# Performance work log

Hardware: AMD Instinct MI355X
Metric: run time of the kernel (lower is better)

## Reference

```python
import jax, jax.numpy as jnp
import numpy as np

B, S, D, H = 2, 2048, 1024, 16
DK = D // H


def setup_inputs() -> dict:
    key = jax.random.key(0)
    ks = jax.random.split(key, 12)
    sc = 1.0 / np.sqrt(D)
    return {
        "q": jax.random.normal(ks[0], (B, S, D), jnp.float32),
        "k": jax.random.normal(ks[1], (B, S, D), jnp.float32),
        "v": jax.random.normal(ks[2], (B, S, D), jnp.float32),
        "mask": jax.random.randint(ks[3], (B, S), 0, 2, jnp.int32),
        "Wq": jax.random.normal(ks[4], (D, D), jnp.float32) * sc,
        "bq": jnp.zeros((D,), jnp.float32),
        "Wk": jax.random.normal(ks[5], (D, D), jnp.float32) * sc,
        "bk": jnp.zeros((D,), jnp.float32),
        "Wv": jax.random.normal(ks[6], (D, D), jnp.float32) * sc,
        "bv": jnp.zeros((D,), jnp.float32),
        "Wo": jax.random.normal(ks[7], (D, D), jnp.float32) * sc,
        "bo": jnp.zeros((D,), jnp.float32),
    }


def reference(q, k, v, mask, Wq, bq, Wk, bk, Wv, bv, Wo, bo):
    # Projections (flax nn.Dense: x @ W + b)
    query = q @ Wq + bq          # [B,S,D]
    key_ = k @ Wk + bk
    value = v @ Wv + bv
    # split heads -> [B,H,S,DK]
    def split(x):
        return x.reshape(B, S, H, DK).transpose(0, 2, 1, 3)
    qh, kh, vh = split(query), split(key_), split(value)
    scores = jnp.einsum('bhqd,bhkd->bhqk', qh, kh) / jnp.sqrt(jnp.float32(DK))
    # Faithful to source: mask=(mask==0); where(mask==0, -1e10, scores)
    # i.e. positions where ORIGINAL mask != 0 are set to -1e10.
    m = (mask == 0)[:, None, None, :]          # [B,1,1,S] bool
    scores = jnp.where(~m, jnp.float32(-1e10), scores)
    attn = jax.nn.softmax(scores, axis=-1)     # dropout deterministic (eval)
    x = jnp.einsum('bhqk,bhkd->bhqd', attn, vh)
    x = x.transpose(0, 2, 1, 3).reshape(B, S, D)
    return x @ Wo + bo
```

## Files before the change

### kernel.cpp

```cpp
#include <hip/hip_runtime.h>
#include <hip/hip_bf16.h>

typedef unsigned short u16;
typedef unsigned int u32;
typedef __attribute__((ext_vector_type(8))) __bf16 bf16x8;
typedef __attribute__((ext_vector_type(4))) float f32x4;
typedef __attribute__((ext_vector_type(16))) float f32x16;

constexpr int Bz = 2, Sq = 2048, Dm = 1024, Hn = 16, DK = 64;

__device__ __forceinline__ u16 f2bf(float f) {
    u32 u = __builtin_bit_cast(u32, f);
    return (u16)((u + 0x7FFFu + ((u >> 16) & 1u)) >> 16);
}

__device__ __forceinline__ u32 pack_bf16(float a, float b) {
#if __has_builtin(__builtin_amdgcn_cvt_pk_bf16_f32)
    return __builtin_bit_cast(u32, __builtin_amdgcn_cvt_pk_bf16_f32(a, b));
#else
    return (u32)f2bf(a) | ((u32)f2bf(b) << 16);
#endif
}

__device__ __forceinline__ bf16x8 lds_frag(const u16* p) {
    return __builtin_bit_cast(bf16x8, *(const uint4*)p);
}
__device__ __forceinline__ bf16x8 gfrag(const u16* p) {
    return __builtin_bit_cast(bf16x8, *(const uint4*)p);
}
__device__ __forceinline__ int swz(int r) { return (r ^ (r >> 3)) & 7; }

__device__ __forceinline__ void gll16(const u16* g, u16* l) {
    __builtin_amdgcn_global_load_lds(
        (const __attribute__((address_space(1))) void*)g,
        (__attribute__((address_space(3))) void*)l, 16, 0, 0);
}

__global__ __launch_bounds__(256) void mha_prep(
    const float* __restrict__ q, const float* __restrict__ k,
    const float* __restrict__ v,
    const float* __restrict__ w0, const float* __restrict__ w1,
    const float* __restrict__ w2, const float* __restrict__ w3,
    const int* __restrict__ mask,
    u16* __restrict__ qkv_dst, u16* __restrict__ wt_dst,
    float* __restrict__ biasg)
{
    __shared__ float tl[64 * 65];
    const int z = blockIdx.z, tid = threadIdx.x;
    if (z < 3) {
        const float* s = (z == 0) ? q : (z == 1) ? k : v;
        u16* d = qkv_dst + (size_t)z * 4 * 1024 * 1024;
        size_t i = ((size_t)blockIdx.x * 256 + tid) * 8;
        float4 a = *(const float4*)(s + i);
        float4 b = *(const float4*)(s + i + 4);
        *(uint4*)(d + i) = make_uint4(pack_bf16(a.x, a.y), pack_bf16(a.z, a.w),
                                      pack_bf16(b.x, b.y), pack_bf16(b.z, b.w));
        return;
    }
    const int bx = blockIdx.x;
    if (bx > 1024) return;
    if (bx == 1024) {
#pragma unroll
        for (int u = 0; u < 4; u++) {
            int4 mm = ((const int4*)mask)[tid * 4 + u];
            float4 bb;
            bb.x = mm.x ? -1.44269504e10f : 0.f;
            bb.y = mm.y ? -1.44269504e10f : 0.f;
            bb.z = mm.z ? -1.44269504e10f : 0.f;
            bb.w = mm.w ? -1.44269504e10f : 0.f;
            ((float4*)biasg)[tid * 4 + u] = bb;
        }
        return;
    }
    const int zi = bx >> 8, t = bx & 255, tr = t >> 4, tc = t & 15;
    const float* src = (zi == 0) ? w0 : (zi == 1) ? w1 : (zi == 2) ? w2 : w3;
    u16* d = wt_dst + (size_t)zi * Dm * Dm;
    {
        int r = tid >> 2, cq = (tid & 3) * 16;
        const float* sp = src + (size_t)(tr * 64 + r) * Dm + tc * 64 + cq;
#pragma unroll
        for (int j = 0; j < 4; j++) {
            float4 vv = *(const float4*)(sp + j * 4);
            tl[r * 65 + cq + j * 4 + 0] = vv.x;
            tl[r * 65 + cq + j * 4 + 1] = vv.y;
            tl[r * 65 + cq + j * 4 + 2] = vv.z;
            tl[r * 65 + cq + j * 4 + 3] = vv.w;
        }
    }
    __syncthreads();
    {
        int rr = tid >> 2, cc = (tid & 3) * 16;
        u16* dp = d + (size_t)(tc * 64 + rr) * Dm + tr * 64 + cc;
        u32 px[8];
#pragma unroll
        for (int j = 0; j < 8; j++)
            px[j] = pack_bf16(tl[(cc + 2 * j) * 65 + rr], tl[(cc + 2 * j + 1) * 65 + rr]);
        *(uint4*)dp       = make_uint4(px[0], px[1], px[2], px[3]);
        *(uint4*)(dp + 8) = make_uint4(px[4], px[5], px[6], px[7]);
    }
}

template<int NI>
__device__ __forceinline__ void gemm_core_dma64(
    const u16* __restrict__ Ab, const u16* __restrict__ Bb,
    u16* As, u16* Bs, f32x4 (&acc)[4][NI])
{
    const int tid = threadIdx.x, lane = tid & 63;
    const int wm = (tid >> 7) & 1, wn = (tid >> 6) & 1;
    const int frow = lane & 15, quad = lane >> 4;

#pragma unroll
    for (int mi = 0; mi < 4; mi++)
#pragma unroll
        for (int ni = 0; ni < NI; ni++) acc[mi][ni] = (f32x4){0.f, 0.f, 0.f, 0.f};

    for (int k0 = 0; k0 < 1024; k0 += 64) {
#pragma unroll
        for (int i = 0; i < 4; i++) {
            int id = tid + i * 256, r = id >> 3, c = id & 7;
            gll16(Ab + (size_t)r * 1024 + k0 + (c ^ swz(r)) * 8, As + (size_t)id * 8);
        }
#pragma unroll
        for (int i = 0; i < NI; i++) {
            int id = tid + i * 256, r = id >> 3, c = id & 7;
            gll16(Bb + (size_t)r * 1024 + k0 + (c ^ swz(r)) * 8, Bs + (size_t)id * 8);
        }
        __syncthreads();
#pragma unroll
        for (int ks = 0; ks < 2; ks++) {
            bf16x8 af[4], bfr[NI];
#pragma unroll
            for (int mi = 0; mi < 4; mi++) {
                int r = wm * 64 + mi * 16 + frow;
                af[mi] = lds_frag(As + r * 64 + ((ks * 4 + quad) ^ swz(r)) * 8);
            }
#pragma unroll
            for (int ni = 0; ni < NI; ni++) {
                int r = wn * (NI * 16) + ni * 16 + frow;
                bfr[ni] = lds_frag(Bs + r * 64 + ((ks * 4 + quad) ^ swz(r)) * 8);
            }
#pragma unroll
            for (int mi = 0; mi < 4; mi++)
#pragma unroll
                for (int ni = 0; ni < NI; ni++)
                    acc[mi][ni] = __builtin_amdgcn_mfma_f32_16x16x32_bf16(
                        af[mi], bfr[ni], acc[mi][ni], 0, 0, 0);
        }
        __syncthreads();
    }
}

__global__ __launch_bounds__(256) void mha_proj_qkv(
    const u16* __restrict__ Qb, const u16* __restrict__ Kb, const u16* __restrict__ Vb,
    const u16* __restrict__ Wqt, const u16* __restrict__ Wkt, const u16* __restrict__ Wvt,
    const float* __restrict__ bq, const float* __restrict__ bk, const float* __restrict__ bv,
    u16* __restrict__ Qh, u16* __restrict__ Kh, u16* __restrict__ Vt)
{
    __shared__ __align__(16) u16 As[128 * 64];
    __shared__ __align__(16) u16 Bs[128 * 64];
    const int z = blockIdx.z, bx = blockIdx.x;
    const u16* Ab; const u16* Bb; const float* bias;
    int m0, n0;
    if (z < 2) {
        m0 = (bx >> 3) * 128; n0 = (bx & 7) * 128;
        Ab = ((z == 0) ? Qb : Kb) + (size_t)m0 * Dm;
        Bb = ((z == 0) ? Wqt : Wkt) + (size_t)n0 * Dm;
        bias = (z == 0) ? bq : bk;
    } else {
        m0 = (bx & 7) * 128; n0 = (bx >> 3) * 128;
        Ab = Wvt + (size_t)m0 * Dm;
        Bb = Vb + (size_t)n0 * Dm;
        bias = bv;
    }

    f32x4 acc[4][4];
    gemm_core_dma64<4>(Ab, Bb, As, Bs, acc);

    const int tid = threadIdx.x, lane = tid & 63;
    const int wm = (tid >> 7) & 1, wn = (tid >> 6) & 1;
    const int frow = lane & 15, quad = lane >> 4;
    u16* dstq = (z == 0) ? Qh : Kh;
#pragma unroll
    for (int mi = 0; mi < 4; mi++)
#pragma unroll
        for (int ni = 0; ni < 4; ni++)
#pragma unroll
            for (int r = 0; r < 4; r++) {
                int i = m0 + wm * 64 + mi * 16 + quad * 4 + r;
                int j = n0 + wn * 64 + ni * 16 + frow;
                if (z < 2) {
                    float val = acc[mi][ni][r] + bias[j];
                    int b = i >> 11, s = i & (Sq - 1);
                    int h = j >> 6, dk = j & (DK - 1);
                    dstq[((size_t)(b * Hn + h) * Sq + s) * DK + dk] = f2bf(val);
                } else {
                    float val = acc[mi][ni][r] + bias[i];
                    int h = i >> 6, dk = i & (DK - 1);
                    int b = j >> 11, s = j & (Sq - 1);
                    int sp = (s & ~12) | ((s & 4) << 1) | ((s & 8) >> 1);
                    Vt[((size_t)(b * Hn + h) * DK + dk) * Sq + sp] = f2bf(val);
                }
            }
}

__global__ __launch_bounds__(512, 4) void mha_attn(
    const u16* __restrict__ Qh, const u16* __restrict__ Kh, const u16* __restrict__ Vt,
    const float* __restrict__ biasg, u16* __restrict__ X)
{
    const int bh = blockIdx.x;
    const int b = bh >> 4;
    const int q0 = blockIdx.y * 64;
    const int tid = threadIdx.x, lane = tid & 63, w = tid >> 6;
    const int wq = w & 1, p = w >> 1;
    const int qc = lane & 31, half = lane >> 5;
    constexpr float C2 = 0.125f * 1.44269504f;

    __shared__ __align__(16) u16 Ks[128 * 64];
    __shared__ __align__(16) u16 Vs[64 * 128];
    __shared__ float lsl[128];

    const u16* Qp = Qh + (size_t)bh * Sq * DK;
    const u16* Kp = Kh + (size_t)bh * Sq * DK;
    const u16* Vp = Vt + (size_t)bh * DK * Sq;
    const float* bp = biasg + b * Sq;

    bf16x8 qf[4];
    {
        const u16* qrow = Qp + (size_t)(q0 + wq * 32 + qc) * DK + half * 8;
#pragma unroll
        for (int kc = 0; kc < 4; kc++) qf[kc] = gfrag(qrow + kc * 16);
    }

    float l_l = 0.f;
    f32x16 o0, o1;
#pragma unroll
    for (int i = 0; i < 16; i++) { o0[i] = 0.f; o1[i] = 0.f; }

    for (int it = 0; it < 16; it++) {
        const int kb = it * 128;
#pragma unroll
        for (int i = 0; i < 2; i++) {
            int id = tid + i * 512;
            int kr = id >> 3, kc_ = id & 7;
            gll16(Kp + (size_t)(kb + kr) * DK + (kc_ ^ swz(kr)) * 8, Ks + (size_t)id * 8);
            int vr = id >> 4, vc = id & 15;
            gll16(Vp + (size_t)vr * Sq + kb + ((vc ^ (vr & 15)) * 8), Vs + (size_t)id * 8);
        }
        __syncthreads();

        const int kr = p * 32 + qc;
        const int K0 = kb + p * 32;
        f32x16 sT;
#pragma unroll
        for (int i = 0; i < 16; i++) sT[i] = 0.f;
#pragma unroll
        for (int kc = 0; kc < 4; kc++) {
            bf16x8 ka = lds_frag(Ks + kr * 64 + ((kc * 2 + half) ^ swz(kr)) * 8);
            sT = __builtin_amdgcn_mfma_f32_32x32x16_bf16(ka, qf[kc], sT, 0, 0, 0);
        }

        float t[16], rs = 0.f;
#pragma unroll
        for (int g = 0; g < 4; g++) {
            float4 mb = *(const float4*)(bp + K0 + 8 * g + 4 * half);
#pragma unroll
            for (int r = 0; r < 4; r++) {
                float bb = (r == 0) ? mb.x : (r == 1) ? mb.y : (r == 2) ? mb.z : mb.w;
                float a = __builtin_amdgcn_exp2f(fmaf(sT[g * 4 + r], C2, bb));
                t[g * 4 + r] = a; rs += a;
            }
        }
        l_l += rs;

        u32 pk[8];
#pragma unroll
        for (int i = 0; i < 8; i++) pk[i] = pack_bf16(t[2 * i], t[2 * i + 1]);

#pragma unroll
        for (int kc = 0; kc < 2; kc++) {
            bf16x8 pf = __builtin_bit_cast(bf16x8,
                make_uint4(pk[4 * kc], pk[4 * kc + 1], pk[4 * kc + 2], pk[4 * kc + 3]));
            int ch = p * 4 + kc * 2 + half;
            bf16x8 va0 = lds_frag(Vs + qc * 128 + ((ch ^ (qc & 15)) * 8));
            bf16x8 va1 = lds_frag(Vs + (32 + qc) * 128 + ((ch ^ ((32 + qc) & 15)) * 8));
            o0 = __builtin_amdgcn_mfma_f32_32x32x16_bf16(va0, pf, o0, 0, 0, 0);
            o1 = __builtin_amdgcn_mfma_f32_32x32x16_bf16(va1, pf, o1, 0, 0, 0);
        }
        __syncthreads();
    }

    l_l += __shfl_xor(l_l, 32);
    float* fc = (float*)Ks + wq * 2048;
#pragma unroll 1
    for (int src = 1; src < 4; src++) {
        if (p == src) {
#pragma unroll
            for (int r = 0; r < 16; r++) fc[r * 64 + lane] = o0[r];
#pragma unroll
            for (int r = 0; r < 16; r++) fc[(16 + r) * 64 + lane] = o1[r];
            lsl[wq * 64 + lane] = l_l;
        }
        __syncthreads();
        if (p == 0) {
#pragma unroll
            for (int r = 0; r < 16; r++) o0[r] += fc[r * 64 + lane];
#pragma unroll
            for (int r = 0; r < 16; r++) o1[r] += fc[(16 + r) * 64 + lane];
            l_l += lsl[wq * 64 + lane];
        }
        __syncthreads();
    }
    if (p == 0) {
        float inv = 1.0f / l_l;
        const int qg = q0 + wq * 32 + qc;
        u16* Xp = X + (size_t)(b * Sq + qg) * Dm + (bh & 15) * DK;
#pragma unroll
        for (int g = 0; g < 4; g++) {
            *(uint2*)&Xp[8 * g + 4 * half] =
                make_uint2(pack_bf16(o0[g * 4 + 0] * inv, o0[g * 4 + 1] * inv),
                           pack_bf16(o0[g * 4 + 2] * inv, o0[g * 4 + 3] * inv));
            *(uint2*)&Xp[32 + 8 * g + 4 * half] =
                make_uint2(pack_bf16(o1[g * 4 + 0] * inv, o1[g * 4 + 1] * inv),
                           pack_bf16(o1[g * 4 + 2] * inv, o1[g * 4 + 3] * inv));
        }
    }
}

__global__ __launch_bounds__(256) void mha_oproj(
    const u16* __restrict__ X, const u16* __restrict__ Wot,
    const float* __restrict__ bo, float* __restrict__ out)
{
    __shared__ __align__(16) u16 As[128 * 64];
    __shared__ __align__(16) u16 Bs[64 * 64];
    const int m0 = blockIdx.y * 128, n0 = blockIdx.x * 64;
    f32x4 acc[4][2];
    gemm_core_dma64<2>(X + (size_t)m0 * Dm, Wot + (size_t)n0 * Dm, As, Bs, acc);
    const int tid = threadIdx.x, lane = tid & 63;
    const int wm = (tid >> 7) & 1, wn = (tid >> 6) & 1;
    const int frow = lane & 15, quad = lane >> 4;
#pragma unroll
    for (int mi = 0; mi < 4; mi++)
#pragma unroll
        for (int ni = 0; ni < 2; ni++)
#pragma unroll
            for (int r = 0; r < 4; r++) {
                int m = m0 + wm * 64 + mi * 16 + quad * 4 + r;
                int n = n0 + wn * 32 + ni * 16 + frow;
                out[(size_t)m * Dm + n] = acc[mi][ni][r] + bo[n];
            }
}

extern "C" void kernel_launch(void* const* d_in, const int* in_sizes, int n_in,
                              void* d_out, int out_size, void* d_ws, size_t ws_size,
                              hipStream_t stream)
{
    const float* qin  = (const float*)d_in[0];
    const float* kin  = (const float*)d_in[1];
    const float* vin  = (const float*)d_in[2];
    const int*   mask = (const int*)d_in[3];
    const float* Wq   = (const float*)d_in[4];
    const float* bq   = (const float*)d_in[5];
    const float* Wk   = (const float*)d_in[6];
    const float* bk   = (const float*)d_in[7];
    const float* Wv   = (const float*)d_in[8];
    const float* bv   = (const float*)d_in[9];
    const float* Wo   = (const float*)d_in[10];
    const float* bo   = (const float*)d_in[11];
    float* out = (float*)d_out;

    u16* ws = (u16*)d_ws;
    const size_t MW = (size_t)Dm * Dm;
    const size_t MT = (size_t)Bz * Sq * Dm;
    u16* Wqt = ws;
    u16* Wkt = ws + MW;
    u16* Wvt = ws + 2 * MW;
    u16* Wot = ws + 3 * MW;
    u16* Qb  = ws + 4 * MW;
    u16* Kb  = Qb + MT;
    u16* Vb  = Kb + MT;
    u16* Qh  = Vb + MT;
    u16* Kh  = Qh + MT;
    u16* Vt  = Kh + MT;
    float* biasg = (float*)(Vt + MT);
    u16* X   = Qb;

    hipLaunchKernelGGL(mha_prep, dim3(2048, 1, 4), dim3(256), 0, stream,
                       qin, kin, vin, Wq, Wk, Wv, Wo, mask, Qb, Wqt, biasg);
    hipLaunchKernelGGL(mha_proj_qkv, dim3(256, 1, 3), dim3(256), 0, stream,
                       Qb, Kb, Vb, Wqt, Wkt, Wvt, bq, bk, bv, Qh, Kh, Vt);
    hipLaunchKernelGGL(mha_attn, dim3(32, 32), dim3(512), 0, stream,
                       Qh, Kh, Vt, biasg, X);
    hipLaunchKernelGGL(mha_oproj, dim3(16, 32), dim3(256), 0, stream,
                       X, Wot, bo, out);
}
```

Before: 255.5 us.

## Shrink QKV projection tiles, double attention KV tile, reorder GEMM block mapping

The QKV projection GEMM now uses 128x64 tiles instead of 128x128, doubling its block count to 1536 so more blocks are resident across CUs. The attention kernel stages 256 keys per iteration instead of 128, halving the number of barrier rounds, at the cost of twice the LDS per block, which may reduce occupancy. Both GEMMs switch to a 1D grid where consecutive blocks share the same weight tile, aiming for better L2 reuse.

```diff
diff --git a/kernel.cpp b/kernel.cpp
--- a/kernel.cpp
+++ b/kernel.cpp
@@ -100,10 +100,9 @@
     }
 }
 
-template<int NI>
-__device__ __forceinline__ void gemm_core_dma64(
+__device__ __forceinline__ void gemm_core_12864(
     const u16* __restrict__ Ab, const u16* __restrict__ Bb,
-    u16* As, u16* Bs, f32x4 (&acc)[4][NI])
+    u16* As, u16* Bs, f32x4 (&acc)[4][2])
 {
     const int tid = threadIdx.x, lane = tid & 63;
     const int wm = (tid >> 7) & 1, wn = (tid >> 6) & 1;
@@ -112,7 +111,7 @@
 #pragma unroll
     for (int mi = 0; mi < 4; mi++)
 #pragma unroll
-        for (int ni = 0; ni < NI; ni++) acc[mi][ni] = (f32x4){0.f, 0.f, 0.f, 0.f};
+        for (int ni = 0; ni < 2; ni++) acc[mi][ni] = (f32x4){0.f, 0.f, 0.f, 0.f};
 
     for (int k0 = 0; k0 < 1024; k0 += 64) {
 #pragma unroll
@@ -121,28 +120,28 @@
             gll16(Ab + (size_t)r * 1024 + k0 + (c ^ swz(r)) * 8, As + (size_t)id * 8);
         }
 #pragma unroll
-        for (int i = 0; i < NI; i++) {
+        for (int i = 0; i < 2; i++) {
             int id = tid + i * 256, r = id >> 3, c = id & 7;
             gll16(Bb + (size_t)r * 1024 + k0 + (c ^ swz(r)) * 8, Bs + (size_t)id * 8);
         }
         __syncthreads();
 #pragma unroll
         for (int ks = 0; ks < 2; ks++) {
-            bf16x8 af[4], bfr[NI];
+            bf16x8 af[4], bfr[2];
 #pragma unroll
             for (int mi = 0; mi < 4; mi++) {
                 int r = wm * 64 + mi * 16 + frow;
                 af[mi] = lds_frag(As + r * 64 + ((ks * 4 + quad) ^ swz(r)) * 8);
             }
 #pragma unroll
-            for (int ni = 0; ni < NI; ni++) {
-                int r = wn * (NI * 16) + ni * 16 + frow;
+            for (int ni = 0; ni < 2; ni++) {
+                int r = wn * 32 + ni * 16 + frow;
                 bfr[ni] = lds_frag(Bs + r * 64 + ((ks * 4 + quad) ^ swz(r)) * 8);
             }
 #pragma unroll
             for (int mi = 0; mi < 4; mi++)
 #pragma unroll
-                for (int ni = 0; ni < NI; ni++)
+                for (int ni = 0; ni < 2; ni++)
                     acc[mi][ni] = __builtin_amdgcn_mfma_f32_16x16x32_bf16(
                         af[mi], bfr[ni], acc[mi][ni], 0, 0, 0);
         }
@@ -157,24 +156,26 @@
     u16* __restrict__ Qh, u16* __restrict__ Kh, u16* __restrict__ Vt)
 {
     __shared__ __align__(16) u16 As[128 * 64];
-    __shared__ __align__(16) u16 Bs[128 * 64];
+    __shared__ __align__(16) u16 Bs[64 * 64];
     const int z = blockIdx.z, bx = blockIdx.x;
     const u16* Ab; const u16* Bb; const float* bias;
     int m0, n0;
     if (z < 2) {
-        m0 = (bx >> 3) * 128; n0 = (bx & 7) * 128;
+        m0 = (bx & 31) * 128;
+        n0 = (bx >> 5) * 64;
         Ab = ((z == 0) ? Qb : Kb) + (size_t)m0 * Dm;
         Bb = ((z == 0) ? Wqt : Wkt) + (size_t)n0 * Dm;
         bias = (z == 0) ? bq : bk;
     } else {
-        m0 = (bx & 7) * 128; n0 = (bx >> 3) * 128;
+        m0 = (bx >> 6) * 128;
+        n0 = (bx & 63) * 64;
         Ab = Wvt + (size_t)m0 * Dm;
         Bb = Vb + (size_t)n0 * Dm;
         bias = bv;
     }
 
-    f32x4 acc[4][4];
-    gemm_core_dma64<4>(Ab, Bb, As, Bs, acc);
+    f32x4 acc[4][2];
+    gemm_core_12864(Ab, Bb, As, Bs, acc);
 
     const int tid = threadIdx.x, lane = tid & 63;
     const int wm = (tid >> 7) & 1, wn = (tid >> 6) & 1;
@@ -183,11 +184,11 @@
 #pragma unroll
     for (int mi = 0; mi < 4; mi++)
 #pragma unroll
-        for (int ni = 0; ni < 4; ni++)
+        for (int ni = 0; ni < 2; ni++)
 #pragma unroll
             for (int r = 0; r < 4; r++) {
                 int i = m0 + wm * 64 + mi * 16 + quad * 4 + r;
-                int j = n0 + wn * 64 + ni * 16 + frow;
+                int j = n0 + wn * 32 + ni * 16 + frow;
                 if (z < 2) {
                     float val = acc[mi][ni][r] + bias[j];
                     int b = i >> 11, s = i & (Sq - 1);
@@ -215,8 +216,8 @@
     const int qc = lane & 31, half = lane >> 5;
     constexpr float C2 = 0.125f * 1.44269504f;
 
-    __shared__ __align__(16) u16 Ks[128 * 64];
-    __shared__ __align__(16) u16 Vs[64 * 128];
+    __shared__ __align__(16) u16 Ks[256 * 64];
+    __shared__ __align__(16) u16 Vs[64 * 256];
     __shared__ float lsl[128];
 
     const u16* Qp = Qh + (size_t)bh * Sq * DK;
@@ -236,55 +237,58 @@
 #pragma unroll
     for (int i = 0; i < 16; i++) { o0[i] = 0.f; o1[i] = 0.f; }
 
-    for (int it = 0; it < 16; it++) {
-        const int kb = it * 128;
-#pragma unroll
-        for (int i = 0; i < 2; i++) {
+    for (int it = 0; it < 8; it++) {
+        const int kb = it * 256;
+#pragma unroll
+        for (int i = 0; i < 4; i++) {
             int id = tid + i * 512;
             int kr = id >> 3, kc_ = id & 7;
             gll16(Kp + (size_t)(kb + kr) * DK + (kc_ ^ swz(kr)) * 8, Ks + (size_t)id * 8);
-            int vr = id >> 4, vc = id & 15;
-            gll16(Vp + (size_t)vr * Sq + kb + ((vc ^ (vr & 15)) * 8), Vs + (size_t)id * 8);
-        }
-        __syncthreads();
-
-        const int kr = p * 32 + qc;
-        const int K0 = kb + p * 32;
-        f32x16 sT;
-#pragma unroll
-        for (int i = 0; i < 16; i++) sT[i] = 0.f;
-#pragma unroll
-        for (int kc = 0; kc < 4; kc++) {
-            bf16x8 ka = lds_frag(Ks + kr * 64 + ((kc * 2 + half) ^ swz(kr)) * 8);
-            sT = __builtin_amdgcn_mfma_f32_32x32x16_bf16(ka, qf[kc], sT, 0, 0, 0);
-        }
-
-        float t[16], rs = 0.f;
-#pragma unroll
-        for (int g = 0; g < 4; g++) {
-            float4 mb = *(const float4*)(bp + K0 + 8 * g + 4 * half);
-#pragma unroll
-            for (int r = 0; r < 4; r++) {
-                float bb = (r == 0) ? mb.x : (r == 1) ? mb.y : (r == 2) ? mb.z : mb.w;
-                float a = __builtin_amdgcn_exp2f(fmaf(sT[g * 4 + r], C2, bb));
-                t[g * 4 + r] = a; rs += a;
-            }
-        }
-        l_l += rs;
-
-        u32 pk[8];
-#pragma unroll
-        for (int i = 0; i < 8; i++) pk[i] = pack_bf16(t[2 * i], t[2 * i + 1]);
-
-#pragma unroll
-        for (int kc = 0; kc < 2; kc++) {
-            bf16x8 pf = __builtin_bit_cast(bf16x8,
-                make_uint4(pk[4 * kc], pk[4 * kc + 1], pk[4 * kc + 2], pk[4 * kc + 3]));
-            int ch = p * 4 + kc * 2 + half;
-            bf16x8 va0 = lds_frag(Vs + qc * 128 + ((ch ^ (qc & 15)) * 8));
-            bf16x8 va1 = lds_frag(Vs + (32 + qc) * 128 + ((ch ^ ((32 + qc) & 15)) * 8));
-            o0 = __builtin_amdgcn_mfma_f32_32x32x16_bf16(va0, pf, o0, 0, 0, 0);
-            o1 = __builtin_amdgcn_mfma_f32_32x32x16_bf16(va1, pf, o1, 0, 0, 0);
+            int vr = id >> 5, vc = id & 31;
+            gll16(Vp + (size_t)vr * Sq + kb + ((vc ^ (vr & 31)) * 8), Vs + (size_t)id * 8);
+        }
+        __syncthreads();
+
+#pragma unroll
+        for (int s = 0; s < 2; s++) {
+            const int kr = p * 64 + s * 32 + qc;
+            const int K0 = kb + p * 64 + s * 32;
+            f32x16 sT;
+#pragma unroll
+            for (int i = 0; i < 16; i++) sT[i] = 0.f;
+#pragma unroll
+            for (int kc = 0; kc < 4; kc++) {
+                bf16x8 ka = lds_frag(Ks + kr * 64 + ((kc * 2 + half) ^ swz(kr)) * 8);
+                sT = __builtin_amdgcn_mfma_f32_32x32x16_bf16(ka, qf[kc], sT, 0, 0, 0);
+            }
+
+            float t[16], rs = 0.f;
+#pragma unroll
+            for (int g = 0; g < 4; g++) {
+                float4 mb = *(const float4*)(bp + K0 + 8 * g + 4 * half);
+#pragma unroll
+                for (int r = 0; r < 4; r++) {
+                    float bb = (r == 0) ? mb.x : (r == 1) ? mb.y : (r == 2) ? mb.z : mb.w;
+                    float a = __builtin_amdgcn_exp2f(fmaf(sT[g * 4 + r], C2, bb));
+                    t[g * 4 + r] = a; rs += a;
+                }
+            }
+            l_l += rs;
+
+            u32 pk[8];
+#pragma unroll
+            for (int i = 0; i < 8; i++) pk[i] = pack_bf16(t[2 * i], t[2 * i + 1]);
+
+#pragma unroll
+            for (int kc = 0; kc < 2; kc++) {
+                bf16x8 pf = __builtin_bit_cast(bf16x8,
+                    make_uint4(pk[4 * kc], pk[4 * kc + 1], pk[4 * kc + 2], pk[4 * kc + 3]));
+                int ch = p * 8 + s * 4 + kc * 2 + half;
+                bf16x8 va0 = lds_frag(Vs + qc * 256 + ((ch ^ (qc & 31)) * 8));
+                bf16x8 va1 = lds_frag(Vs + (32 + qc) * 256 + ((ch ^ ((32 + qc) & 31)) * 8));
+                o0 = __builtin_amdgcn_mfma_f32_32x32x16_bf16(va0, pf, o0, 0, 0, 0);
+                o1 = __builtin_amdgcn_mfma_f32_32x32x16_bf16(va1, pf, o1, 0, 0, 0);
+            }
         }
         __syncthreads();
     }
@@ -332,9 +336,10 @@
 {
     __shared__ __align__(16) u16 As[128 * 64];
     __shared__ __align__(16) u16 Bs[64 * 64];
-    const int m0 = blockIdx.y * 128, n0 = blockIdx.x * 64;
+    const int bx = blockIdx.x;
+    const int m0 = (bx & 31) * 128, n0 = (bx >> 5) * 64;
     f32x4 acc[4][2];
-    gemm_core_dma64<2>(X + (size_t)m0 * Dm, Wot + (size_t)n0 * Dm, As, Bs, acc);
+    gemm_core_12864(X + (size_t)m0 * Dm, Wot + (size_t)n0 * Dm, As, Bs, acc);
     const int tid = threadIdx.x, lane = tid & 63;
     const int wm = (tid >> 7) & 1, wn = (tid >> 6) & 1;
     const int frow = lane & 15, quad = lane >> 4;
@@ -386,10 +391,10 @@
 
     hipLaunchKernelGGL(mha_prep, dim3(2048, 1, 4), dim3(256), 0, stream,
                        qin, kin, vin, Wq, Wk, Wv, Wo, mask, Qb, Wqt, biasg);
-    hipLaunchKernelGGL(mha_proj_qkv, dim3(256, 1, 3), dim3(256), 0, stream,
+    hipLaunchKernelGGL(mha_proj_qkv, dim3(512, 1, 3), dim3(256), 0, stream,
                        Qb, Kb, Vb, Wqt, Wkt, Wvt, bq, bk, bv, Qh, Kh, Vt);
     hipLaunchKernelGGL(mha_attn, dim3(32, 32), dim3(512), 0, stream,
                        Qh, Kh, Vt, biasg, X);
-    hipLaunchKernelGGL(mha_oproj, dim3(16, 32), dim3(256), 0, stream,
+    hipLaunchKernelGGL(mha_oproj, dim3(512), dim3(256), 0, stream,
                        X, Wot, bo, out);
 }
```

After: 252.3 us. No clear change (-1.2%).
